# Kernel tuning notes

Measured on AMD Instinct MI355X. Metric: run time of the kernel, lower is better.

The kernel has to match this reference:

```python
import jax, jax.numpy as jnp
import numpy as np
from math import factorial

# module hyperparameters (match init_kwargs)
IN_FEATURES = 512
TAU_0 = 0.1
DT = 0.1
K = 4
C = 0.1
ALPHA = 1.0
G = 0
NTAU = 400
T_EVERY = 4
SEQ = 512


def _build_constants():
    """Replicates _calc_tau_star / _calc_D / _calc_invL in float64 numpy."""
    n = NTAU + 2 * K  # 408
    tau_star = TAU_0 * (1.0 + C) ** np.arange(-K, NTAU + K, dtype=np.float64)
    s = K / tau_star
    s0 = s[1:-1] - s[:-2]
    s1 = s[2:] - s[1:-1]
    s11 = s[2:] - s[:-2]
    A = -(s1 / s11 / s0)
    B = -(s0 / s11 / s1) + s1 / s11 / s0
    Cc = s0 / s11 / s1
    D = np.zeros((n, n), dtype=np.float64)
    r = np.arange(n - 2)
    D[r + 1, r] = A
    D[r + 1, r + 1] = B
    D[r + 1, r + 2] = Cc
    D = D.T
    invL = ((-1.0) ** K / factorial(K)
            * (np.linalg.matrix_power(D, K) @ np.diag(s ** (K + 1.0))))[:, K:-K].T  # [ntau, n]
    e_alph_dt = np.exp(-s * ALPHA * DT)
    decay = (1.0 / (ALPHA * s)) * (1.0 - e_alph_dt)          # [n]
    d = e_alph_dt ** (TAU_0 / DT)                             # per-step decay (dur = tau_0)
    subset = tau_star[K:-K:T_EVERY] ** G                      # [O]
    invL_sub = invL[::T_EVERY]                                # [O, n] (slice commutes with matmul rows)
    return invL_sub, d, decay, subset


def setup_inputs() -> dict:
    key = jax.random.key(0)
    invL_sub, d, decay, subset = _build_constants()
    inp = jax.random.normal(key, (SEQ, IN_FEATURES), dtype=jnp.float32)
    return {
        "inp": inp,
        "invL_sub": jnp.asarray(invL_sub, jnp.float32),
        "d": jnp.asarray(d, jnp.float32),
        "decay": jnp.asarray(decay, jnp.float32),
        "subset": jnp.asarray(subset, jnp.float32),
    }


def reference(inp, invL_sub, d, decay, subset):
    # t_{c} = diag(e^{-s*alpha*dt})^{dur/dt} t_{c-1} + decay * alpha * inp_c * (dur/dt)
    scale = TAU_0 / DT  # dur/dt with dur defaulting to tau_0
    u = (decay * ALPHA * scale)[None, :, None] * inp[:, None, :]  # [T, n, F]

    def step(t, u_t):
        t_new = d[:, None] * t + u_t
        return t_new, t_new

    t0 = jnp.zeros((d.shape[0], inp.shape[1]), inp.dtype)
    _, ts = jax.lax.scan(step, t0, u)  # [T, n, F]
    # output[c] = (invL @ t_c)[::T_every] * subset_tau_star  (invL rows pre-sliced)
    out = jnp.einsum('on,tnf->tof', invL_sub, ts) * subset[None, :, None]
    return out
```

## Files before the change

kernel.cpp:

```cpp
#include <hip/hip_runtime.h>


#define NF   512
#define NN   408
#define NO   100
#define NC   16
#define TC   32
#define NB   15
#define TAPS 9
#define OPG  5
#define NG   20
#define ROWS 25
#define NPT  4

__global__ __launch_bounds__(256) void sith_pass1(
    const float* __restrict__ inp, const float* __restrict__ d,
    float* __restrict__ P)
{
    int fs = blockIdx.x;
    int a  = blockIdx.y;
    int b  = blockIdx.z;
    int tid = threadIdx.x;
    int lane = tid & 63;
    int y = tid >> 6;
    int n0 = a * 16 + y * NPT;
    if (n0 >= NN) return;
    int f = fs * 64 + lane;

    float dreg[NPT], st[NPT];
    #pragma unroll
    for (int q = 0; q < NPT; ++q) {
        dreg[q] = d[n0 + q];
        st[q] = 0.f;
    }

    const float* ip = inp + b * TC * NF + f;
    #pragma unroll
    for (int tt = 0; tt < TC; tt += 8) {
        float x[8];
        #pragma unroll
        for (int u = 0; u < 8; ++u)
            x[u] = ip[(tt + u) * NF];
        #pragma unroll
        for (int u = 0; u < 8; ++u) {
            #pragma unroll
            for (int q = 0; q < NPT; ++q)
                st[q] = fmaf(dreg[q], st[q], x[u]);
        }
    }
    #pragma unroll
    for (int q = 0; q < NPT; ++q)
        P[b * (NN * NF) + (n0 + q) * NF + f] = st[q];
}

__global__ __launch_bounds__(128) void sith_pass2(
    const float* __restrict__ inp, const float* __restrict__ invL,
    const float* __restrict__ d, const float* __restrict__ decay,
    const float* __restrict__ subset, const float* __restrict__ P,
    float* __restrict__ out)
{
    int bx = blockIdx.x;
    int fs = bx & 7;
    int oc = bx >> 3;
    int c  = blockIdx.y;
    int tid = threadIdx.x;
    int lane = tid & 63;
    int w = tid >> 6;
    int g = oc * 2 + w;
    int f = fs * 64 + lane;
    int nbase = NG * g;

    float dreg[ROWS], p[ROWS];
    #pragma unroll
    for (int j = 0; j < ROWS; ++j)
        dreg[j] = d[nbase + j];

    if (c == 0) {
        #pragma unroll
        for (int j = 0; j < ROWS; ++j) p[j] = 0.f;
    } else {
        float d32[ROWS];
        #pragma unroll
        for (int j = 0; j < ROWS; ++j) {
            float d2 = dreg[j] * dreg[j];
            float d4 = d2 * d2, d8 = d4 * d4, d16 = d8 * d8;
            d32[j] = d16 * d16;
        }
        const float* Pb = P + nbase * NF + f;
        #pragma unroll
        for (int j = 0; j < ROWS; ++j)
            p[j] = Pb[j * NF];
        for (int k = 1; k < c; ++k) {
            const float* Pk = Pb + k * (NN * NF);
            #pragma unroll
            for (int j = 0; j < ROWS; ++j)
                p[j] = fmaf(d32[j], p[j], Pk[j * NF]);
        }
    }

    float L[OPG][TAPS];
    #pragma unroll
    for (int k = 0; k < OPG; ++k) {
        int o = OPG * g + k;
        float sub = subset[o];
        #pragma unroll
        for (int dd = 0; dd < TAPS; ++dd) {
            int n = nbase + 4 * k + dd;
            L[k][dd] = invL[o * NN + n] * sub * decay[n];
        }
    }

    const float* ip = inp + f;
    int t0 = c * TC;
    int obase = (t0 * NO + OPG * g) * NF + f;

#define SITH_STEP(s, xv)                                                   \
    {                                                                      \
        _Pragma("unroll")                                                  \
        for (int j = 0; j < ROWS; ++j)                                     \
            p[j] = fmaf(dreg[j], p[j], (xv));                              \
        _Pragma("unroll")                                                  \
        for (int k = 0; k < OPG; ++k) {                                    \
            float a0 = 0.f;                                                \
            _Pragma("unroll")                                              \
            for (int dd = 0; dd < TAPS; ++dd)                              \
                a0 = fmaf(L[k][dd], p[4 * k + dd], a0);                    \
            acc[s][k] = a0;                                                \
        }                                                                  \
    }

    float xb0 = ip[(t0 + 0) * NF];
    float xb1 = ip[(t0 + 1) * NF];
    float xb2 = ip[(t0 + 2) * NF];
    float xb3 = ip[(t0 + 3) * NF];

    for (int tq = 0; tq < TC; tq += 4) {
        int tp = t0 + tq + 4;
        float xn0 = ip[((tp + 0) & 511) * NF];
        float xn1 = ip[((tp + 1) & 511) * NF];
        float xn2 = ip[((tp + 2) & 511) * NF];
        float xn3 = ip[((tp + 3) & 511) * NF];

        float acc[4][OPG];
        SITH_STEP(0, xb0);
        SITH_STEP(1, xb1);
        SITH_STEP(2, xb2);
        SITH_STEP(3, xb3);

        #pragma unroll
        for (int s = 0; s < 4; ++s) {
            #pragma unroll
            for (int k = 0; k < OPG; ++k)
                __builtin_nontemporal_store(acc[s][k],
                    &out[obase + (s * NO + k) * NF]);
        }
        obase += 4 * NO * NF;

        xb0 = xn0; xb1 = xn1; xb2 = xn2; xb3 = xn3;
    }
#undef SITH_STEP
}

extern "C" void kernel_launch(void* const* d_in, const int* in_sizes, int n_in,
                              void* d_out, int out_size, void* d_ws, size_t ws_size,
                              hipStream_t stream)
{
    const float* inp    = (const float*)d_in[0];
    const float* invL   = (const float*)d_in[1];
    const float* d      = (const float*)d_in[2];
    const float* decay  = (const float*)d_in[3];
    const float* subset = (const float*)d_in[4];
    float* out = (float*)d_out;
    float* P   = (float*)d_ws;

    sith_pass1<<<dim3(8, 26, NB), 256, 0, stream>>>(inp, d, P);
    sith_pass2<<<dim3(80, NC), 128, 0, stream>>>(inp, invL, d, decay, subset, P, out);
}
```

Baseline: 37.53 us.

## Add carry-prefix kernel and stage outputs through LDS for vectorized stores

Adds a separate kernel that runs the chunk-carry recurrence across the 15 chunk partials once, so pass2 loads a single precomputed state instead of each block looping over up to c previous chunks. Pass2 is reorganized into 512-thread blocks covering all 512 features for one output group. Results are staged through double-buffered shared memory and written back as float4 stores. This trades one extra kernel launch and a __syncthreads per 4 timesteps for less redundant carry work and wider global stores. It also drops the nontemporal store hint.

```diff
diff --git a/kernel.cpp b/kernel.cpp
--- a/kernel.cpp
+++ b/kernel.cpp
@@ -13,7 +13,7 @@
 #define ROWS 25
 #define NPT  4
 
-__global__ __launch_bounds__(256) void sith_pass1(
+__global__ __launch_bounds__(256) void sith_pass1a(
     const float* __restrict__ inp, const float* __restrict__ d,
     float* __restrict__ P)
 {
@@ -33,14 +33,12 @@
         dreg[q] = d[n0 + q];
         st[q] = 0.f;
     }
-
     const float* ip = inp + b * TC * NF + f;
     #pragma unroll
     for (int tt = 0; tt < TC; tt += 8) {
         float x[8];
         #pragma unroll
-        for (int u = 0; u < 8; ++u)
-            x[u] = ip[(tt + u) * NF];
+        for (int u = 0; u < 8; ++u) x[u] = ip[(tt + u) * NF];
         #pragma unroll
         for (int u = 0; u < 8; ++u) {
             #pragma unroll
@@ -53,49 +51,50 @@
         P[b * (NN * NF) + (n0 + q) * NF + f] = st[q];
 }
 
-__global__ __launch_bounds__(128) void sith_pass2(
+__global__ __launch_bounds__(256) void sith_pass1b(
+    const float* __restrict__ d, float* __restrict__ P)
+{
+    int fs = blockIdx.x;
+    int n  = blockIdx.y * 4 + (threadIdx.x >> 6);
+    int f  = fs * 64 + (threadIdx.x & 63);
+    float dn = d[n];
+    float d2 = dn * dn, d4 = d2 * d2, d8 = d4 * d4, d16 = d8 * d8;
+    float d32 = d16 * d16;
+
+    float* Pb = P + n * NF + f;
+    float v[NB];
+    #pragma unroll
+    for (int b = 0; b < NB; ++b) v[b] = Pb[b * (NN * NF)];
+    float acc = v[0];
+    #pragma unroll
+    for (int b = 1; b < NB; ++b) {
+        acc = fmaf(d32, acc, v[b]);
+        Pb[b * (NN * NF)] = acc;
+    }
+}
+
+__global__ __launch_bounds__(512) void sith_pass2(
     const float* __restrict__ inp, const float* __restrict__ invL,
     const float* __restrict__ d, const float* __restrict__ decay,
     const float* __restrict__ subset, const float* __restrict__ P,
     float* __restrict__ out)
 {
-    int bx = blockIdx.x;
-    int fs = bx & 7;
-    int oc = bx >> 3;
-    int c  = blockIdx.y;
+    __shared__ float lds[2][20][NF];
+
+    int g = blockIdx.x;
+    int c = blockIdx.y;
     int tid = threadIdx.x;
     int lane = tid & 63;
     int w = tid >> 6;
-    int g = oc * 2 + w;
-    int f = fs * 64 + lane;
+    int f = w * 64 + lane;
     int nbase = NG * g;
 
     float dreg[ROWS], p[ROWS];
     #pragma unroll
-    for (int j = 0; j < ROWS; ++j)
-        dreg[j] = d[nbase + j];
-
-    if (c == 0) {
-        #pragma unroll
-        for (int j = 0; j < ROWS; ++j) p[j] = 0.f;
-    } else {
-        float d32[ROWS];
-        #pragma unroll
-        for (int j = 0; j < ROWS; ++j) {
-            float d2 = dreg[j] * dreg[j];
-            float d4 = d2 * d2, d8 = d4 * d4, d16 = d8 * d8;
-            d32[j] = d16 * d16;
-        }
-        const float* Pb = P + nbase * NF + f;
-        #pragma unroll
-        for (int j = 0; j < ROWS; ++j)
-            p[j] = Pb[j * NF];
-        for (int k = 1; k < c; ++k) {
-            const float* Pk = Pb + k * (NN * NF);
-            #pragma unroll
-            for (int j = 0; j < ROWS; ++j)
-                p[j] = fmaf(d32[j], p[j], Pk[j * NF]);
-        }
+    for (int j = 0; j < ROWS; ++j) {
+        int n = nbase + j;
+        dreg[j] = d[n];
+        p[j] = (c == 0) ? 0.f : P[(c - 1) * (NN * NF) + n * NF + f];
     }
 
     float L[OPG][TAPS];
@@ -112,7 +111,8 @@
 
     const float* ip = inp + f;
     int t0 = c * TC;
-    int obase = (t0 * NO + OPG * g) * NF + f;
+    int srow = tid >> 7;
+    int f4   = (tid & 127) << 2;
 
 #define SITH_STEP(s, xv)                                                   \
     {                                                                      \
@@ -147,14 +147,24 @@
         SITH_STEP(2, xb2);
         SITH_STEP(3, xb3);
 
+        int buf = (tq >> 2) & 1;
         #pragma unroll
-        for (int s = 0; s < 4; ++s) {
+        for (int s = 0; s < 4; ++s)
             #pragma unroll
             for (int k = 0; k < OPG; ++k)
-                __builtin_nontemporal_store(acc[s][k],
-                    &out[obase + (s * NO + k) * NF]);
+                lds[buf][s * OPG + k][f] = acc[s][k];
+
+        __syncthreads();
+
+        #pragma unroll
+        for (int r = 0; r < 5; ++r) {
+            int row = r * 4 + srow;
+            int s   = row / OPG;
+            int k   = row - s * OPG;
+            float4 v = *reinterpret_cast<const float4*>(&lds[buf][row][f4]);
+            *reinterpret_cast<float4*>(
+                &out[((t0 + tq + s) * NO + OPG * g + k) * NF + f4]) = v;
         }
-        obase += 4 * NO * NF;
 
         xb0 = xn0; xb1 = xn1; xb2 = xn2; xb3 = xn3;
     }
@@ -173,6 +183,7 @@
     float* out = (float*)d_out;
     float* P   = (float*)d_ws;
 
-    sith_pass1<<<dim3(8, 26, NB), 256, 0, stream>>>(inp, d, P);
-    sith_pass2<<<dim3(80, NC), 128, 0, stream>>>(inp, invL, d, decay, subset, P, out);
+    sith_pass1a<<<dim3(8, 26, NB), 256, 0, stream>>>(inp, d, P);
+    sith_pass1b<<<dim3(8, 102), 256, 0, stream>>>(d, P);
+    sith_pass2<<<dim3(NG, NC), 512, 0, stream>>>(inp, invL, d, decay, subset, P, out);
 }
```

New measurement: 51.00 us. 1.36x slower.
